# Kernel optimization log

Measured on AMD Instinct MI355X. Metric: run time of the kernel, lower is better.

Reference implementation:

```python
import jax, jax.numpy as jnp
import numpy as np

REG_MAX = 16
BOX_W = 7.5
OBJ_W = 1.0
TOPK = 10
EPS = 1e-7


def dfl_decode(x, reg_max):
    # x: [B, 4*reg_max, N] -> expected value of per-side distribution -> [B, N, 4] (xyxy)
    B, C, N = x.shape
    x = x.reshape(B, 4, reg_max, N)
    p = jax.nn.softmax(x, axis=2)
    proj = jnp.arange(reg_max, dtype=x.dtype)
    return jnp.einsum('bkrn,r->bnk', p, proj)


def bbox_ciou(b1, b2):
    # b1: [B,N,1,4], b2: [B,1,M,4], xyxy -> [B,N,M]
    x11, y11, x12, y12 = b1[..., 0], b1[..., 1], b1[..., 2], b1[..., 3]
    x21, y21, x22, y22 = b2[..., 0], b2[..., 1], b2[..., 2], b2[..., 3]
    w1, h1 = x12 - x11, y12 - y11
    w2, h2 = x22 - x21, y22 - y21
    iw = jnp.clip(jnp.minimum(x12, x22) - jnp.maximum(x11, x21), 0.0)
    ih = jnp.clip(jnp.minimum(y12, y22) - jnp.maximum(y11, y21), 0.0)
    inter = iw * ih
    union = w1 * h1 + w2 * h2 - inter + EPS
    iou = inter / union
    cw = jnp.maximum(x12, x22) - jnp.minimum(x11, x21)
    ch = jnp.maximum(y12, y22) - jnp.minimum(y11, y21)
    c2 = cw * cw + ch * ch + EPS
    rho2 = ((x21 + x22 - x11 - x12) ** 2 + (y21 + y22 - y11 - y12) ** 2) * 0.25
    v = (4.0 / (np.pi ** 2)) * (jnp.arctan(w2 / (h2 + EPS)) - jnp.arctan(w1 / (h1 + EPS))) ** 2
    alpha = jax.lax.stop_gradient(v / (v - iou + 1.0 + EPS))
    return iou - rho2 / c2 - alpha * v


def setup_inputs() -> dict:
    key = jax.random.key(0)
    k1, k2, k3, k4 = jax.random.split(key, 4)
    B, N, M = 8, 34000, 64
    boxes = jax.random.normal(k1, (B, 4 * REG_MAX, N), dtype=jnp.float32)
    scores = jax.random.normal(k2, (B, N), dtype=jnp.float32)
    # GT boxes: valid xyxy in roughly the same [0, reg_max) range as decoded preds
    xy = jax.random.uniform(k3, (B, M, 2), dtype=jnp.float32) * 11.0
    wh = jax.random.uniform(k4, (B, M, 2), dtype=jnp.float32) * 4.0 + 0.5
    targets = jnp.concatenate([xy, xy + wh], axis=-1)
    return {'boxes': boxes, 'scores': scores, 'targets': targets}


def reference(boxes, scores, targets):
    B, N = scores.shape
    M = targets.shape[1]
    pb = dfl_decode(boxes, REG_MAX)                     # [B,N,4]
    ciou = bbox_ciou(pb[:, :, None, :], targets[:, None, :, :])  # [B,N,M]
    k = min(TOPK, N)
    topv, topi = jax.lax.top_k(jnp.swapaxes(ciou, 1, 2), k)      # [B,M,k] over anchors
    valid = topv > 0.0
    vals = jnp.where(valid, topv, 0.0)

    def per_batch(idx, val, vld):
        flat_i = idx.reshape(-1)
        iou_t = jnp.zeros((N,), val.dtype).at[flat_i].max(val.reshape(-1))
        pos = jnp.zeros((N,), bool).at[flat_i].max(vld.reshape(-1))
        return iou_t, pos

    iou_target, pos = jax.vmap(per_batch)(topi, vals, valid)     # [B,N]
    posf = pos.astype(iou_target.dtype)
    npos = posf.sum(axis=1)
    box_per = jnp.where(npos > 0,
                        ((1.0 - iou_target) * posf).sum(axis=1) / jnp.maximum(npos, 1.0),
                        0.0)
    box_loss = box_per.sum()
    # BCEWithLogits (mean over anchors), summed over batch
    bce = jnp.maximum(scores, 0.0) - scores * iou_target + jnp.log1p(jnp.exp(-jnp.abs(scores)))
    obj_loss = bce.mean(axis=1).sum()
    total = (BOX_W * box_loss + OBJ_W * obj_loss) / B
    return total, box_loss, obj_loss
```

## Files before the change

kernel.cpp:

```cpp
#include <hip/hip_runtime.h>
#include <math.h>

#define BQ 8
#define MQ 64
#define REGMAX 16
#define KTOP 10
#define EPSQ 1e-7f
#define APB 256
#define MBUF 1344

__device__ __forceinline__ float frcp(float x) { return __builtin_amdgcn_rcpf(x); }

__device__ __forceinline__ float dfl_side(const float* __restrict__ p, size_t Ns) {
  float x0 = p[0];
  float x1 = p[Ns];
  float x2 = p[2 * Ns];
  float x3 = p[3 * Ns];
  float x4 = p[4 * Ns];
  float x5 = p[5 * Ns];
  float x6 = p[6 * Ns];
  float x7 = p[7 * Ns];
  float x8 = p[8 * Ns];
  float x9 = p[9 * Ns];
  float x10 = p[10 * Ns];
  float x11 = p[11 * Ns];
  float x12 = p[12 * Ns];
  float x13 = p[13 * Ns];
  float x14 = p[14 * Ns];
  float x15 = p[15 * Ns];
  float mx = fmaxf(fmaxf(fmaxf(fmaxf(x0, x1), fmaxf(x2, x3)),
                         fmaxf(fmaxf(x4, x5), fmaxf(x6, x7))),
                   fmaxf(fmaxf(fmaxf(x8, x9), fmaxf(x10, x11)),
                         fmaxf(fmaxf(x12, x13), fmaxf(x14, x15))));
  float s = 0.f, ws = 0.f, e;
  e = __expf(x0 - mx); s += e;
  e = __expf(x1 - mx); s += e; ws += 1.f * e;
  e = __expf(x2 - mx); s += e; ws += 2.f * e;
  e = __expf(x3 - mx); s += e; ws += 3.f * e;
  e = __expf(x4 - mx); s += e; ws += 4.f * e;
  e = __expf(x5 - mx); s += e; ws += 5.f * e;
  e = __expf(x6 - mx); s += e; ws += 6.f * e;
  e = __expf(x7 - mx); s += e; ws += 7.f * e;
  e = __expf(x8 - mx); s += e; ws += 8.f * e;
  e = __expf(x9 - mx); s += e; ws += 9.f * e;
  e = __expf(x10 - mx); s += e; ws += 10.f * e;
  e = __expf(x11 - mx); s += e; ws += 11.f * e;
  e = __expf(x12 - mx); s += e; ws += 12.f * e;
  e = __expf(x13 - mx); s += e; ws += 13.f * e;
  e = __expf(x14 - mx); s += e; ws += 14.f * e;
  e = __expf(x15 - mx); s += e; ws += 15.f * e;
  return ws * frcp(s);
}

__global__ __launch_bounds__(256, 4) void decode_topk_kernel(
    const float* __restrict__ boxes, const float* __restrict__ scores,
    const float* __restrict__ targets, unsigned int* __restrict__ iou_bits,
    uint2* __restrict__ cand, float* __restrict__ bcePartial,
    unsigned int* __restrict__ ctr, int N, int bpb) {
  const int tid = threadIdx.x;
  const int b = blockIdx.x / bpb;
  const int blk = blockIdx.x - b * bpb;
  const int a0 = blk * APB;
  const int w = tid >> 6;
  const int l = tid & 63;

  __shared__ float4 s_sv[APB];
  __shared__ float s_at[APB];
  __shared__ int s_ix[APB];
  __shared__ float s_hv[4 * MQ * KTOP];
  __shared__ int s_hi[4 * MQ * KTOP];
  __shared__ uint2 s_mg[MQ * KTOP];
  __shared__ int s_cnt;
  __shared__ float s_bce;
  if (tid == 0) { s_cnt = 0; s_bce = 0.f; }
  if (blockIdx.x == 0 && tid == 0) *ctr = 0u;
  __syncthreads();

  const int n = a0 + tid;
  float bce0 = 0.f;
  bool pred = false;
  float e0 = 0.f, e1 = 0.f, e2 = 0.f, e3 = 0.f, at = 0.f;
  if (n < N) {
    const size_t i = (size_t)b * N + n;
    iou_bits[i] = 0u;
    float sc = scores[i];
    bce0 = fmaxf(sc, 0.f) + log1pf(__expf(-fabsf(sc)));
    const size_t Ns = (size_t)N;
    const float* base = boxes + (size_t)(b * 64) * Ns + n;
    e0 = dfl_side(base, Ns);
    e1 = dfl_side(base + 16 * Ns, Ns);
    e2 = dfl_side(base + 32 * Ns, Ns);
    e3 = dfl_side(base + 48 * Ns, Ns);
    float w1 = e2 - e0, h1 = e3 - e1;
    if (w1 > 0.f && h1 > 0.f) {
      pred = true;
      at = atanf(w1 * frcp(h1 + EPSQ));
    }
  }
  {
    unsigned long long mask = __ballot(pred);
    int cnt = __popcll(mask);
    int bslot = 0;
    if (l == 0 && cnt) bslot = atomicAdd(&s_cnt, cnt);
    bslot = __shfl(bslot, 0, 64);
    if (pred) {
      int pos = bslot + __popcll(mask & ((1ull << l) - 1ull));
      s_sv[pos] = make_float4(e0, e1, e2, e3);
      s_at[pos] = at;
      s_ix[pos] = n;
    }
  }
#pragma unroll
  for (int d = 1; d < 64; d <<= 1) bce0 += __shfl_xor(bce0, d, 64);
  if (l == 0) atomicAdd(&s_bce, bce0);
  __syncthreads();
  const int nsurv = s_cnt;
  if (tid == 0) bcePartial[blockIdx.x] = s_bce;

  const float4 t = ((const float4*)targets)[b * MQ + l];
  const float x21 = t.x, y21 = t.y, x22 = t.z, y22 = t.w;
  const float w2 = x22 - x21, h2 = y22 - y21;
  const float atan_t = atanf(w2 * frcp(h2 + EPSQ));
  const float area2 = w2 * h2, sumx2 = x21 + x22, sumy2 = y21 + y22;
  const float CPI = 4.0f / (float)(M_PI * M_PI);

  float hv0 = 0.f, hv1 = 0.f, hv2 = 0.f, hv3 = 0.f, hv4 = 0.f;
  float hv5 = 0.f, hv6 = 0.f, hv7 = 0.f, hv8 = 0.f, hv9 = 0.f;
  int hi0 = 0, hi1 = 0, hi2 = 0, hi3 = 0, hi4 = 0;
  int hi5 = 0, hi6 = 0, hi7 = 0, hi8 = 0, hi9 = 0;

  const int qlen = (nsurv + 3) >> 2;
  const int j0 = w * qlen;
  const int j1 = min(nsurv, j0 + qlen);
  for (int j = j0; j < j1; ++j) {
    float4 p = s_sv[j];
    float pa = s_at[j];
    int ixj = s_ix[j];
    float x11 = p.x, y11 = p.y, x12 = p.z, y12 = p.w;
    float w1 = x12 - x11, h1 = y12 - y11;
    float iw = fmaxf(fminf(x12, x22) - fmaxf(x11, x21), 0.f);
    float ih = fmaxf(fminf(y12, y22) - fmaxf(y11, y21), 0.f);
    float inter = iw * ih;
    float uni = w1 * h1 + area2 - inter + EPSQ;
    float iou = inter * frcp(uni);
    float cw = fmaxf(x12, x22) - fminf(x11, x21);
    float ch = fmaxf(y12, y22) - fminf(y11, y21);
    float c2 = cw * cw + ch * ch + EPSQ;
    float dx = sumx2 - x11 - x12;
    float dy = sumy2 - y11 - y12;
    float rho2 = (dx * dx + dy * dy) * 0.25f;
    float da = atan_t - pa;
    float v = CPI * da * da;
    float alpha = v * frcp(v - iou + 1.f + EPSQ);
    float ciou = iou - rho2 * frcp(c2) - alpha * v;
    if (ciou > hv9) {
      float cv = ciou;
      int ci = ixj;
#define INS(vk, ik)                         \
  {                                         \
    bool gt = cv > vk;                      \
    float tv_ = vk; int ti_ = ik;           \
    vk = gt ? cv : vk; ik = gt ? ci : ik;   \
    cv = gt ? tv_ : cv; ci = gt ? ti_ : ci; \
  }
      INS(hv0, hi0) INS(hv1, hi1) INS(hv2, hi2) INS(hv3, hi3) INS(hv4, hi4)
      INS(hv5, hi5) INS(hv6, hi6) INS(hv7, hi7) INS(hv8, hi8) INS(hv9, hi9)
#undef INS
    }
  }
  const int hb = (w * MQ + l) * KTOP;
  s_hv[hb + 0] = hv0; s_hi[hb + 0] = hi0;
  s_hv[hb + 1] = hv1; s_hi[hb + 1] = hi1;
  s_hv[hb + 2] = hv2; s_hi[hb + 2] = hi2;
  s_hv[hb + 3] = hv3; s_hi[hb + 3] = hi3;
  s_hv[hb + 4] = hv4; s_hi[hb + 4] = hi4;
  s_hv[hb + 5] = hv5; s_hi[hb + 5] = hi5;
  s_hv[hb + 6] = hv6; s_hi[hb + 6] = hi6;
  s_hv[hb + 7] = hv7; s_hi[hb + 7] = hi7;
  s_hv[hb + 8] = hv8; s_hi[hb + 8] = hi8;
  s_hv[hb + 9] = hv9; s_hi[hb + 9] = hi9;
  __syncthreads();

  if (w == 0) {
    const int m = l;
    int p0 = 0, p1 = 0, p2 = 0, p3 = 0;
    for (int r = 0; r < KTOP; ++r) {
      float c0 = s_hv[(0 * MQ + m) * KTOP + p0];
      float c1 = s_hv[(1 * MQ + m) * KTOP + p1];
      float c2m = s_hv[(2 * MQ + m) * KTOP + p2];
      float c3 = s_hv[(3 * MQ + m) * KTOP + p3];
      float best = c0; int bw = 0;
      if (c1 > best) { best = c1; bw = 1; }
      if (c2m > best) { best = c2m; bw = 2; }
      if (c3 > best) { best = c3; bw = 3; }
      int psel = (bw == 0) ? p0 : (bw == 1) ? p1 : (bw == 2) ? p2 : p3;
      int bidx = s_hi[(bw * MQ + m) * KTOP + psel];
      s_mg[m * KTOP + r] = make_uint2(__float_as_uint(best), (unsigned)bidx);
      if (bw == 0) p0 = min(p0 + 1, KTOP - 1);
      else if (bw == 1) p1 = min(p1 + 1, KTOP - 1);
      else if (bw == 2) p2 = min(p2 + 1, KTOP - 1);
      else p3 = min(p3 + 1, KTOP - 1);
    }
  }
  __syncthreads();
  for (int sl = tid; sl < MQ * KTOP; sl += 256) {
    int m = sl / KTOP;
    int r = sl - m * KTOP;
    cand[((size_t)(b * MQ + m) * bpb + blk) * KTOP + r] = s_mg[sl];
  }
}

__device__ __forceinline__ void select_top10(
    float* s_bv, int* s_bi, float* s_winv, int* s_wini,
    int* s_cnt, int c, int tid) {
  if (tid < 64) {
    for (int r = 0; r < KTOP; ++r) {
      float bv = 0.f;
      int bs = 0xffff;
      for (int sl = tid; sl < c; sl += 64) {
        float v = s_bv[sl];
        if (v > bv) { bv = v; bs = sl; }
      }
      unsigned long long key =
          ((unsigned long long)__float_as_uint(bv) << 32) | (unsigned int)bs;
#pragma unroll
      for (int d = 1; d < 64; d <<= 1) {
        unsigned long long o = __shfl_xor(key, d, 64);
        if (o > key) key = o;
      }
      if (tid == 0) {
        float wv = __uint_as_float((unsigned int)(key >> 32));
        int ws = (int)(key & 0xffffu);
        s_winv[r] = wv;
        if (wv > 0.f && ws != 0xffff) {
          s_wini[r] = s_bi[ws];
          s_bv[ws] = 0.f;
        } else {
          s_wini[r] = 0;
        }
      }
    }
    if (tid < KTOP) { s_bv[tid] = s_winv[tid]; s_bi[tid] = s_wini[tid]; }
    if (tid == 0) *s_cnt = KTOP;
  }
}

__global__ __launch_bounds__(256) void merge_kernel(
    const uint2* __restrict__ cand, const float* __restrict__ scores,
    unsigned int* __restrict__ iou_bits, const float* __restrict__ bcePartial,
    float* __restrict__ mergePartial, unsigned int* __restrict__ ctr,
    float* __restrict__ out, int N, int bpb) {
  const int bm = blockIdx.x;
  const int b = bm >> 6;
  const int tid = threadIdx.x;
  const int l = tid & 63;
  const int NC = bpb * KTOP;

  __shared__ float s_bv[MBUF];
  __shared__ int s_bi[MBUF];
  __shared__ float s_winv[KTOP];
  __shared__ int s_wini[KTOP];
  __shared__ int s_cnt;
  __shared__ float s_d[3];
  __shared__ int s_last;
  __shared__ float s_acc[BQ * 3];
  if (tid == 0) s_cnt = 0;
  if (tid < 3) s_d[tid] = 0.f;
  if (tid < BQ * 3) s_acc[tid] = 0.f;
  __syncthreads();

  const uint2* cbase = cand + (size_t)bm * NC;
  for (int k2 = tid; k2 < NC; k2 += 256) {
    uint2 e = cbase[k2];
    float v = __uint_as_float(e.x);
    bool p = v > 0.f;
    unsigned long long mask = __ballot(p);
    int cnt = __popcll(mask);
    int bslot = 0;
    if (l == 0 && cnt) bslot = atomicAdd(&s_cnt, cnt);
    bslot = __shfl(bslot, 0, 64);
    if (p) {
      int pos = bslot + __popcll(mask & ((1ull << l) - 1ull));
      s_bv[pos] = v;
      s_bi[pos] = (int)e.y;
    }
  }
  __syncthreads();
  int c = s_cnt;
  __syncthreads();
  if (c > KTOP) {
    select_top10(s_bv, s_bi, s_winv, s_wini, &s_cnt, c, tid);
    __syncthreads();
    c = KTOP;
  }
  if (tid < KTOP && tid < c) {
    float v = s_bv[tid];
    if (v > 0.f) {
      int ix = s_bi[tid];
      unsigned int vb = __float_as_uint(v);
      unsigned int old = atomicMax(&iou_bits[(size_t)b * N + ix], vb);
      if (old < vb) {
        float vold = __uint_as_float(old);
        bool was = (old != 0u);
        atomicAdd(&s_d[0], was ? (vold - v) : (1.f - v));
        if (!was) atomicAdd(&s_d[1], 1.f);
        atomicAdd(&s_d[2], -scores[(size_t)b * N + ix] * (v - vold));
      }
    }
  }
  __syncthreads();
  if (tid == 0) {
    float4* mp = (float4*)(mergePartial + (size_t)bm * 4);
    *mp = make_float4(s_d[0], s_d[1], s_d[2], 0.f);
    __threadfence();
    unsigned int done = atomicAdd(ctr, 1u);
    s_last = (done == (unsigned)(gridDim.x - 1)) ? 1 : 0;
  }
  __syncthreads();
  if (s_last) {
    __threadfence();
    volatile const float* mp = mergePartial;
    for (int i = tid; i < BQ * MQ; i += 256) {
      int bb = i >> 6;
      float a0 = mp[i * 4 + 0];
      float a1 = mp[i * 4 + 1];
      float a2 = mp[i * 4 + 2];
      atomicAdd(&s_acc[bb * 3 + 0], a0);
      atomicAdd(&s_acc[bb * 3 + 1], a1);
      atomicAdd(&s_acc[bb * 3 + 2], a2);
    }
    volatile const float* bp = bcePartial;
    for (int i = tid; i < BQ * bpb; i += 256) {
      int bb = i / bpb;
      atomicAdd(&s_acc[bb * 3 + 2], bp[i]);
    }
    __syncthreads();
    if (tid == 0) {
      float box = 0.f, obj = 0.f;
      for (int bb = 0; bb < BQ; ++bb) {
        float np = s_acc[bb * 3 + 1];
        box += (np > 0.f) ? s_acc[bb * 3 + 0] / fmaxf(np, 1.f) : 0.f;
        obj += s_acc[bb * 3 + 2] / (float)N;
      }
      out[0] = (7.5f * box + obj) / (float)BQ;
      out[1] = box;
      out[2] = obj;
    }
  }
}

extern "C" void kernel_launch(void* const* d_in, const int* in_sizes, int n_in,
                              void* d_out, int out_size, void* d_ws, size_t ws_size,
                              hipStream_t stream) {
  const float* boxes = (const float*)d_in[0];
  const float* scores = (const float*)d_in[1];
  const float* targets = (const float*)d_in[2];
  float* out = (float*)d_out;
  const int N = in_sizes[1] / BQ;

  const int bpb = (N + APB - 1) / APB;
  const int nblk = BQ * bpb;

  char* ws = (char*)d_ws;
  size_t cand_bytes = (size_t)BQ * MQ * bpb * KTOP * sizeof(uint2);
  size_t iou_bytes = (size_t)BQ * N * sizeof(unsigned int);
  size_t bce_bytes = (((size_t)nblk * sizeof(float)) + 255) & ~(size_t)255;
  size_t mp_bytes = (size_t)BQ * MQ * 4 * sizeof(float);

  uint2* cand = (uint2*)ws;                    ws += cand_bytes;
  unsigned int* iou_bits = (unsigned int*)ws;  ws += iou_bytes;
  float* bcePartial = (float*)ws;              ws += bce_bytes;
  float* mergePartial = (float*)ws;            ws += mp_bytes;
  unsigned int* ctr = (unsigned int*)ws;

  decode_topk_kernel<<<nblk, 256, 0, stream>>>(boxes, scores, targets,
                                               iou_bits, cand, bcePartial, ctr, N, bpb);
  merge_kernel<<<BQ * MQ, 256, 0, stream>>>(cand, scores, iou_bits, bcePartial,
                                            mergePartial, ctr, out, N, bpb);
}
```

Measured before the change: 143.8 us.

## Hoist all 64 DFL loads, drop occupancy hint, transpose candidate buffer layout

All 64 per-anchor DFL logits are now loaded up front before any softmax work, so more memory requests are in flight per thread. The launch-bounds minimum-occupancy hint is removed, letting the compiler use more registers to hold the loaded values. The candidate buffer is changed from [B,M,blk,K] to [B,blk,M,K] order. Decode blocks now write one contiguous run, while the merge kernel reads 10-element strided chunks. The cost is higher register pressure, possibly lower occupancy, and less coalesced merge reads.

```diff
diff --git a/kernel.cpp b/kernel.cpp
--- a/kernel.cpp
+++ b/kernel.cpp
@@ -11,48 +11,40 @@
 
 __device__ __forceinline__ float frcp(float x) { return __builtin_amdgcn_rcpf(x); }
 
-__device__ __forceinline__ float dfl_side(const float* __restrict__ p, size_t Ns) {
-  float x0 = p[0];
-  float x1 = p[Ns];
-  float x2 = p[2 * Ns];
-  float x3 = p[3 * Ns];
-  float x4 = p[4 * Ns];
-  float x5 = p[5 * Ns];
-  float x6 = p[6 * Ns];
-  float x7 = p[7 * Ns];
-  float x8 = p[8 * Ns];
-  float x9 = p[9 * Ns];
-  float x10 = p[10 * Ns];
-  float x11 = p[11 * Ns];
-  float x12 = p[12 * Ns];
-  float x13 = p[13 * Ns];
-  float x14 = p[14 * Ns];
-  float x15 = p[15 * Ns];
-  float mx = fmaxf(fmaxf(fmaxf(fmaxf(x0, x1), fmaxf(x2, x3)),
-                         fmaxf(fmaxf(x4, x5), fmaxf(x6, x7))),
-                   fmaxf(fmaxf(fmaxf(x8, x9), fmaxf(x10, x11)),
-                         fmaxf(fmaxf(x12, x13), fmaxf(x14, x15))));
-  float s = 0.f, ws = 0.f, e;
-  e = __expf(x0 - mx); s += e;
-  e = __expf(x1 - mx); s += e; ws += 1.f * e;
-  e = __expf(x2 - mx); s += e; ws += 2.f * e;
-  e = __expf(x3 - mx); s += e; ws += 3.f * e;
-  e = __expf(x4 - mx); s += e; ws += 4.f * e;
-  e = __expf(x5 - mx); s += e; ws += 5.f * e;
-  e = __expf(x6 - mx); s += e; ws += 6.f * e;
-  e = __expf(x7 - mx); s += e; ws += 7.f * e;
-  e = __expf(x8 - mx); s += e; ws += 8.f * e;
-  e = __expf(x9 - mx); s += e; ws += 9.f * e;
-  e = __expf(x10 - mx); s += e; ws += 10.f * e;
-  e = __expf(x11 - mx); s += e; ws += 11.f * e;
-  e = __expf(x12 - mx); s += e; ws += 12.f * e;
-  e = __expf(x13 - mx); s += e; ws += 13.f * e;
-  e = __expf(x14 - mx); s += e; ws += 14.f * e;
-  e = __expf(x15 - mx); s += e; ws += 15.f * e;
-  return ws * frcp(s);
-}
-
-__global__ __launch_bounds__(256, 4) void decode_topk_kernel(
+#define DECL_LOAD16(P, G)                                                      \
+  float G##0 = (P)[0], G##1 = (P)[Ns], G##2 = (P)[2 * Ns], G##3 = (P)[3 * Ns], \
+        G##4 = (P)[4 * Ns], G##5 = (P)[5 * Ns], G##6 = (P)[6 * Ns],            \
+        G##7 = (P)[7 * Ns], G##8 = (P)[8 * Ns], G##9 = (P)[9 * Ns],            \
+        G##10 = (P)[10 * Ns], G##11 = (P)[11 * Ns], G##12 = (P)[12 * Ns],      \
+        G##13 = (P)[13 * Ns], G##14 = (P)[14 * Ns], G##15 = (P)[15 * Ns];
+
+#define EV16(G, OUT)                                                           \
+  {                                                                            \
+    float mx = fmaxf(fmaxf(fmaxf(fmaxf(G##0, G##1), fmaxf(G##2, G##3)),        \
+                           fmaxf(fmaxf(G##4, G##5), fmaxf(G##6, G##7))),       \
+                     fmaxf(fmaxf(fmaxf(G##8, G##9), fmaxf(G##10, G##11)),      \
+                           fmaxf(fmaxf(G##12, G##13), fmaxf(G##14, G##15))));  \
+    float s = 0.f, ws = 0.f, e;                                                \
+    e = __expf(G##0 - mx); s += e;                                             \
+    e = __expf(G##1 - mx); s += e; ws += 1.f * e;                              \
+    e = __expf(G##2 - mx); s += e; ws += 2.f * e;                              \
+    e = __expf(G##3 - mx); s += e; ws += 3.f * e;                              \
+    e = __expf(G##4 - mx); s += e; ws += 4.f * e;                              \
+    e = __expf(G##5 - mx); s += e; ws += 5.f * e;                              \
+    e = __expf(G##6 - mx); s += e; ws += 6.f * e;                              \
+    e = __expf(G##7 - mx); s += e; ws += 7.f * e;                              \
+    e = __expf(G##8 - mx); s += e; ws += 8.f * e;                              \
+    e = __expf(G##9 - mx); s += e; ws += 9.f * e;                              \
+    e = __expf(G##10 - mx); s += e; ws += 10.f * e;                            \
+    e = __expf(G##11 - mx); s += e; ws += 11.f * e;                            \
+    e = __expf(G##12 - mx); s += e; ws += 12.f * e;                            \
+    e = __expf(G##13 - mx); s += e; ws += 13.f * e;                            \
+    e = __expf(G##14 - mx); s += e; ws += 14.f * e;                            \
+    e = __expf(G##15 - mx); s += e; ws += 15.f * e;                            \
+    OUT = ws * frcp(s);                                                        \
+  }
+
+__global__ __launch_bounds__(256) void decode_topk_kernel(
     const float* __restrict__ boxes, const float* __restrict__ scores,
     const float* __restrict__ targets, unsigned int* __restrict__ iou_bits,
     uint2* __restrict__ cand, float* __restrict__ bcePartial,
@@ -83,14 +75,22 @@
   if (n < N) {
     const size_t i = (size_t)b * N + n;
     iou_bits[i] = 0u;
+    const size_t Ns = (size_t)N;
+    const float* base = boxes + (size_t)(b * 64) * Ns + n;
+    const float* p0 = base;
+    const float* p1 = base + 16 * Ns;
+    const float* p2 = base + 32 * Ns;
+    const float* p3 = base + 48 * Ns;
+    DECL_LOAD16(p0, a)
+    DECL_LOAD16(p1, bv)
+    DECL_LOAD16(p2, c)
+    DECL_LOAD16(p3, d)
     float sc = scores[i];
     bce0 = fmaxf(sc, 0.f) + log1pf(__expf(-fabsf(sc)));
-    const size_t Ns = (size_t)N;
-    const float* base = boxes + (size_t)(b * 64) * Ns + n;
-    e0 = dfl_side(base, Ns);
-    e1 = dfl_side(base + 16 * Ns, Ns);
-    e2 = dfl_side(base + 32 * Ns, Ns);
-    e3 = dfl_side(base + 48 * Ns, Ns);
+    EV16(a, e0)
+    EV16(bv, e1)
+    EV16(c, e2)
+    EV16(d, e3)
     float w1 = e2 - e0, h1 = e3 - e1;
     if (w1 > 0.f && h1 > 0.f) {
       pred = true;
@@ -203,11 +203,8 @@
     }
   }
   __syncthreads();
-  for (int sl = tid; sl < MQ * KTOP; sl += 256) {
-    int m = sl / KTOP;
-    int r = sl - m * KTOP;
-    cand[((size_t)(b * MQ + m) * bpb + blk) * KTOP + r] = s_mg[sl];
-  }
+  uint2* obase = cand + (size_t)(b * bpb + blk) * (MQ * KTOP);
+  for (int sl = tid; sl < MQ * KTOP; sl += 256) obase[sl] = s_mg[sl];
 }
 
 __device__ __forceinline__ void select_top10(
@@ -252,6 +249,7 @@
     float* __restrict__ out, int N, int bpb) {
   const int bm = blockIdx.x;
   const int b = bm >> 6;
+  const int m = bm & 63;
   const int tid = threadIdx.x;
   const int l = tid & 63;
   const int NC = bpb * KTOP;
@@ -269,9 +267,10 @@
   if (tid < BQ * 3) s_acc[tid] = 0.f;
   __syncthreads();
 
-  const uint2* cbase = cand + (size_t)bm * NC;
   for (int k2 = tid; k2 < NC; k2 += 256) {
-    uint2 e = cbase[k2];
+    int blkk = k2 / KTOP;
+    int r = k2 - blkk * KTOP;
+    uint2 e = cand[((size_t)(b * bpb + blkk) * MQ + m) * KTOP + r];
     float v = __uint_as_float(e.x);
     bool p = v > 0.f;
     unsigned long long mask = __ballot(p);
@@ -362,7 +361,7 @@
   const int nblk = BQ * bpb;
 
   char* ws = (char*)d_ws;
-  size_t cand_bytes = (size_t)BQ * MQ * bpb * KTOP * sizeof(uint2);
+  size_t cand_bytes = (size_t)BQ * bpb * MQ * KTOP * sizeof(uint2);
   size_t iou_bytes = (size_t)BQ * N * sizeof(unsigned int);
   size_t bce_bytes = (((size_t)nblk * sizeof(float)) + 255) & ~(size_t)255;
   size_t mp_bytes = (size_t)BQ * MQ * 4 * sizeof(float);
```

Measured after the change: 142.5 us. Within noise of the previous version (-0.9%).

## Split decode from top-k scan and double anchors per top-k block

Applied to the files above, without the earlier changes.

The fused decode+top-k kernel becomes two kernels. One decodes the DFL boxes into a float4 workspace and writes per-wave BCE partials. The other reads 512 anchors per block for the CIoU top-k scan, which halves the number of per-block candidate lists that the merge kernel must scan. This trades an extra global round trip of decoded boxes (about 4 MB) and an extra launch for lighter register and LDS pressure in the decode phase and less merge work. The candidate layout changes to block-major, and the merge kernel's strided reads are adjusted to match.

```diff
diff --git a/kernel.cpp b/kernel.cpp
--- a/kernel.cpp
+++ b/kernel.cpp
@@ -3,10 +3,10 @@
 
 #define BQ 8
 #define MQ 64
-#define REGMAX 16
 #define KTOP 10
 #define EPSQ 1e-7f
-#define APB 256
+#define APBA 256
+#define CHUNK 512
 #define MBUF 1344
 
 __device__ __forceinline__ float frcp(float x) { return __builtin_amdgcn_rcpf(x); }
@@ -52,34 +52,20 @@
   return ws * frcp(s);
 }
 
-__global__ __launch_bounds__(256, 4) void decode_topk_kernel(
+__global__ __launch_bounds__(256) void decode_kernel(
     const float* __restrict__ boxes, const float* __restrict__ scores,
-    const float* __restrict__ targets, unsigned int* __restrict__ iou_bits,
-    uint2* __restrict__ cand, float* __restrict__ bcePartial,
-    unsigned int* __restrict__ ctr, int N, int bpb) {
+    float4* __restrict__ ev4, unsigned int* __restrict__ iou_bits,
+    float* __restrict__ bcePartial, unsigned int* __restrict__ ctr,
+    int N, int bpbA) {
   const int tid = threadIdx.x;
-  const int b = blockIdx.x / bpb;
-  const int blk = blockIdx.x - b * bpb;
-  const int a0 = blk * APB;
+  const int b = blockIdx.x / bpbA;
+  const int blk = blockIdx.x - b * bpbA;
+  const int n = blk * APBA + tid;
   const int w = tid >> 6;
   const int l = tid & 63;
-
-  __shared__ float4 s_sv[APB];
-  __shared__ float s_at[APB];
-  __shared__ int s_ix[APB];
-  __shared__ float s_hv[4 * MQ * KTOP];
-  __shared__ int s_hi[4 * MQ * KTOP];
-  __shared__ uint2 s_mg[MQ * KTOP];
-  __shared__ int s_cnt;
-  __shared__ float s_bce;
-  if (tid == 0) { s_cnt = 0; s_bce = 0.f; }
   if (blockIdx.x == 0 && tid == 0) *ctr = 0u;
-  __syncthreads();
-
-  const int n = a0 + tid;
+
   float bce0 = 0.f;
-  bool pred = false;
-  float e0 = 0.f, e1 = 0.f, e2 = 0.f, e3 = 0.f, at = 0.f;
   if (n < N) {
     const size_t i = (size_t)b * N + n;
     iou_bits[i] = 0u;
@@ -87,17 +73,51 @@
     bce0 = fmaxf(sc, 0.f) + log1pf(__expf(-fabsf(sc)));
     const size_t Ns = (size_t)N;
     const float* base = boxes + (size_t)(b * 64) * Ns + n;
-    e0 = dfl_side(base, Ns);
-    e1 = dfl_side(base + 16 * Ns, Ns);
-    e2 = dfl_side(base + 32 * Ns, Ns);
-    e3 = dfl_side(base + 48 * Ns, Ns);
-    float w1 = e2 - e0, h1 = e3 - e1;
-    if (w1 > 0.f && h1 > 0.f) {
-      pred = true;
-      at = atanf(w1 * frcp(h1 + EPSQ));
-    }
-  }
-  {
+    float e0 = dfl_side(base, Ns);
+    float e1 = dfl_side(base + 16 * Ns, Ns);
+    float e2 = dfl_side(base + 32 * Ns, Ns);
+    float e3 = dfl_side(base + 48 * Ns, Ns);
+    ev4[i] = make_float4(e0, e1, e2, e3);
+  }
+#pragma unroll
+  for (int d = 1; d < 64; d <<= 1) bce0 += __shfl_xor(bce0, d, 64);
+  if (l == 0) bcePartial[blockIdx.x * 4 + w] = bce0;
+}
+
+__global__ __launch_bounds__(256) void topk_kernel(
+    const float4* __restrict__ ev4, const float* __restrict__ targets,
+    uint2* __restrict__ cand, int N, int bpbB) {
+  const int tid = threadIdx.x;
+  const int b = blockIdx.x / bpbB;
+  const int blk = blockIdx.x - b * bpbB;
+  const int c0 = blk * CHUNK;
+  const int w = tid >> 6;
+  const int l = tid & 63;
+
+  __shared__ float4 s_sv[CHUNK];
+  __shared__ float s_at[CHUNK];
+  __shared__ int s_ix[CHUNK];
+  __shared__ float s_hv[4 * MQ * KTOP];
+  __shared__ int s_hi[4 * MQ * KTOP];
+  __shared__ uint2 s_mg[MQ * KTOP];
+  __shared__ int s_cnt;
+  if (tid == 0) s_cnt = 0;
+  __syncthreads();
+
+#pragma unroll
+  for (int p = 0; p < CHUNK / 256; ++p) {
+    const int n = c0 + p * 256 + tid;
+    bool pred = false;
+    float4 ev = make_float4(0.f, 0.f, 0.f, 0.f);
+    float at = 0.f;
+    if (n < N) {
+      ev = ev4[(size_t)b * N + n];
+      float w1 = ev.z - ev.x, h1 = ev.w - ev.y;
+      if (w1 > 0.f && h1 > 0.f) {
+        pred = true;
+        at = atanf(w1 * frcp(h1 + EPSQ));
+      }
+    }
     unsigned long long mask = __ballot(pred);
     int cnt = __popcll(mask);
     int bslot = 0;
@@ -105,17 +125,13 @@
     bslot = __shfl(bslot, 0, 64);
     if (pred) {
       int pos = bslot + __popcll(mask & ((1ull << l) - 1ull));
-      s_sv[pos] = make_float4(e0, e1, e2, e3);
+      s_sv[pos] = ev;
       s_at[pos] = at;
       s_ix[pos] = n;
     }
   }
-#pragma unroll
-  for (int d = 1; d < 64; d <<= 1) bce0 += __shfl_xor(bce0, d, 64);
-  if (l == 0) atomicAdd(&s_bce, bce0);
   __syncthreads();
   const int nsurv = s_cnt;
-  if (tid == 0) bcePartial[blockIdx.x] = s_bce;
 
   const float4 t = ((const float4*)targets)[b * MQ + l];
   const float x21 = t.x, y21 = t.y, x22 = t.z, y22 = t.w;
@@ -185,11 +201,11 @@
     const int m = l;
     int p0 = 0, p1 = 0, p2 = 0, p3 = 0;
     for (int r = 0; r < KTOP; ++r) {
-      float c0 = s_hv[(0 * MQ + m) * KTOP + p0];
+      float c0v = s_hv[(0 * MQ + m) * KTOP + p0];
       float c1 = s_hv[(1 * MQ + m) * KTOP + p1];
       float c2m = s_hv[(2 * MQ + m) * KTOP + p2];
       float c3 = s_hv[(3 * MQ + m) * KTOP + p3];
-      float best = c0; int bw = 0;
+      float best = c0v; int bw = 0;
       if (c1 > best) { best = c1; bw = 1; }
       if (c2m > best) { best = c2m; bw = 2; }
       if (c3 > best) { best = c3; bw = 3; }
@@ -203,11 +219,8 @@
     }
   }
   __syncthreads();
-  for (int sl = tid; sl < MQ * KTOP; sl += 256) {
-    int m = sl / KTOP;
-    int r = sl - m * KTOP;
-    cand[((size_t)(b * MQ + m) * bpb + blk) * KTOP + r] = s_mg[sl];
-  }
+  uint2* obase = cand + (size_t)(b * bpbB + blk) * (MQ * KTOP);
+  for (int sl = tid; sl < MQ * KTOP; sl += 256) obase[sl] = s_mg[sl];
 }
 
 __device__ __forceinline__ void select_top10(
@@ -249,12 +262,13 @@
     const uint2* __restrict__ cand, const float* __restrict__ scores,
     unsigned int* __restrict__ iou_bits, const float* __restrict__ bcePartial,
     float* __restrict__ mergePartial, unsigned int* __restrict__ ctr,
-    float* __restrict__ out, int N, int bpb) {
+    float* __restrict__ out, int N, int bpbB, int bpbA) {
   const int bm = blockIdx.x;
   const int b = bm >> 6;
+  const int m = bm & 63;
   const int tid = threadIdx.x;
   const int l = tid & 63;
-  const int NC = bpb * KTOP;
+  const int NC = bpbB * KTOP;
 
   __shared__ float s_bv[MBUF];
   __shared__ int s_bi[MBUF];
@@ -269,9 +283,10 @@
   if (tid < BQ * 3) s_acc[tid] = 0.f;
   __syncthreads();
 
-  const uint2* cbase = cand + (size_t)bm * NC;
   for (int k2 = tid; k2 < NC; k2 += 256) {
-    uint2 e = cbase[k2];
+    int blkk = k2 / KTOP;
+    int r = k2 - blkk * KTOP;
+    uint2 e = cand[((size_t)(b * bpbB + blkk) * MQ + m) * KTOP + r];
     float v = __uint_as_float(e.x);
     bool p = v > 0.f;
     unsigned long long mask = __ballot(p);
@@ -330,8 +345,9 @@
       atomicAdd(&s_acc[bb * 3 + 2], a2);
     }
     volatile const float* bp = bcePartial;
-    for (int i = tid; i < BQ * bpb; i += 256) {
-      int bb = i / bpb;
+    const int per_b = bpbA * 4;
+    for (int i = tid; i < BQ * per_b; i += 256) {
+      int bb = i / per_b;
       atomicAdd(&s_acc[bb * 3 + 2], bp[i]);
     }
     __syncthreads();
@@ -358,23 +374,28 @@
   float* out = (float*)d_out;
   const int N = in_sizes[1] / BQ;
 
-  const int bpb = (N + APB - 1) / APB;
-  const int nblk = BQ * bpb;
+  const int bpbA = (N + APBA - 1) / APBA;
+  const int nblkA = BQ * bpbA;
+  const int bpbB = (N + CHUNK - 1) / CHUNK;
+  const int nblkB = BQ * bpbB;
 
   char* ws = (char*)d_ws;
-  size_t cand_bytes = (size_t)BQ * MQ * bpb * KTOP * sizeof(uint2);
+  size_t ev_bytes = (size_t)BQ * N * sizeof(float4);
+  size_t cand_bytes = (size_t)BQ * bpbB * MQ * KTOP * sizeof(uint2);
   size_t iou_bytes = (size_t)BQ * N * sizeof(unsigned int);
-  size_t bce_bytes = (((size_t)nblk * sizeof(float)) + 255) & ~(size_t)255;
+  size_t bce_bytes = (((size_t)nblkA * 4 * sizeof(float)) + 255) & ~(size_t)255;
   size_t mp_bytes = (size_t)BQ * MQ * 4 * sizeof(float);
 
+  float4* ev4 = (float4*)ws;                   ws += ev_bytes;
   uint2* cand = (uint2*)ws;                    ws += cand_bytes;
   unsigned int* iou_bits = (unsigned int*)ws;  ws += iou_bytes;
   float* bcePartial = (float*)ws;              ws += bce_bytes;
   float* mergePartial = (float*)ws;            ws += mp_bytes;
   unsigned int* ctr = (unsigned int*)ws;
 
-  decode_topk_kernel<<<nblk, 256, 0, stream>>>(boxes, scores, targets,
-                                               iou_bits, cand, bcePartial, ctr, N, bpb);
+  decode_kernel<<<nblkA, 256, 0, stream>>>(boxes, scores, ev4, iou_bits,
+                                           bcePartial, ctr, N, bpbA);
+  topk_kernel<<<nblkB, 256, 0, stream>>>(ev4, targets, cand, N, bpbB);
   merge_kernel<<<BQ * MQ, 256, 0, stream>>>(cand, scores, iou_bits, bcePartial,
-                                            mergePartial, ctr, out, N, bpb);
-}
+                                            mergePartial, ctr, out, N, bpbB, bpbA);
+}
```

After: 147.9 us. 1.03x slower.
